# Performance work log

Hardware: AMD Instinct MI355X
Metric: run time of the kernel (lower is better)

The kernel has to match this reference:

```python
import jax, jax.numpy as jnp
import numpy as np

EPS = 1e-8

def _layernorm(x, gamma, beta):
    mu = jnp.mean(x, axis=-1, keepdims=True)
    var = jnp.mean((x - mu) ** 2, axis=-1, keepdims=True)
    return (x - mu) * jax.lax.rsqrt(var + 1e-5) * gamma + beta

def setup_inputs() -> dict:
    key = jax.random.key(0)
    ks = jax.random.split(key, 8)
    B, T, E, H = 64, 512, 512, 2048  # T == E required by original matmul
    s = 1.0 / np.sqrt(E)
    return {
        "x": jax.random.normal(ks[0], (B, T, E), dtype=jnp.float32),
        "gamma1": jnp.ones((E,), jnp.float32),
        "beta1": jnp.zeros((E,), jnp.float32),
        "Wv": jax.random.normal(ks[1], (E, E), jnp.float32) * s,   # surrogate for quantum Vx circuit
        "Ww": jax.random.normal(ks[2], (E, E), jnp.float32) * s,   # surrogate for quantum xWx circuit
        "gamma2": jnp.ones((E,), jnp.float32),
        "beta2": jnp.zeros((E,), jnp.float32),
        "W1": jax.random.normal(ks[3], (E, H), jnp.float32) * s,
        "b1": jnp.zeros((H,), jnp.float32),
        "W2": jax.random.normal(ks[4], (H, E), jnp.float32) * (1.0 / np.sqrt(H)),
        "b2": jnp.zeros((E,), jnp.float32),
    }

def reference(x, gamma1, beta1, Wv, Ww, gamma2, beta2, W1, b1, W2, b2):
    # LN -> quantum-surrogate attention -> residual -> LN -> MLP -> residual
    inp = _layernorm(x, gamma1, beta1)                       # [B,T,E]
    # Quantum Vx surrogate: sampler returns probabilities (non-negative) -> squared projection
    vx = (jnp.einsum('bte,ef->btf', inp, Wv)) ** 2           # [B,T,E], >= 0
    # Quantum xWx surrogate: pairwise bilinear score, squared (probability-like)
    proj = jnp.einsum('bte,ef->btf', inp, Ww)                # [B,T,E]
    xwx = (jnp.einsum('bie,bje->bij', proj, inp)) ** 2       # [B,T,T], >= 0
    vx = jnp.sqrt(vx + EPS)
    xwx = jnp.sqrt(xwx + EPS)
    attn = jax.nn.softmax(xwx, axis=-1)                      # [B,T,T]
    # original: matmul(attn, vx.transpose(1,2)) -> out[b,i,k] = sum_j attn[b,i,j] * vx[b,k,j]
    t = jnp.einsum('bij,bkj->bik', attn, vx)                 # [B,T,T] (T == E)
    x = x + t
    h = _layernorm(x, gamma2, beta2)
    h = jax.nn.gelu(jnp.einsum('bte,eh->bth', h, W1) + b1)
    h = jnp.einsum('bth,he->bte', h, W2) + b2
    return x + h
```

## Files before the change

kernel.cpp:

```cpp
#include <hip/hip_runtime.h>

using f16x8 = __attribute__((ext_vector_type(8))) _Float16;
using f32x4 = __attribute__((ext_vector_type(4))) float;
using u16 = unsigned short;
using u32 = unsigned int;

__device__ __forceinline__ u16 f2h(float f) {
  union { _Float16 h; u16 u; } c;
  c.h = (_Float16)f;
  return c.u;
}
__device__ __forceinline__ uint4 pack8(const u16* h) {
  uint4 r;
  r.x = (u32)h[0] | ((u32)h[1] << 16);
  r.y = (u32)h[2] | ((u32)h[3] << 16);
  r.z = (u32)h[4] | ((u32)h[5] << 16);
  r.w = (u32)h[6] | ((u32)h[7] << 16);
  return r;
}
__device__ __forceinline__ float gelu_fast(float x) {
  float u2 = 1.5957691216057308f * (x + 0.044715f * x * x * x);
  return x / (1.0f + __expf(-u2));
}
__device__ __forceinline__ void gload16(const void* g, void* l) {
  __builtin_amdgcn_global_load_lds(
      (const __attribute__((address_space(1))) void*)g,
      (__attribute__((address_space(3))) void*)l, 16, 0, 0);
}

__global__ __launch_bounds__(256) void transpose_f16_kernel(
    const float* __restrict__ in, u16* __restrict__ out, int R, int C)
{
  __shared__ float t[32][33];
  const int lx = threadIdx.x & 31, ly = threadIdx.x >> 5;
  const int c0 = blockIdx.x << 5, r0 = blockIdx.y << 5;
  for (int i = ly; i < 32; i += 8)
    t[i][lx] = in[(long)(r0 + i) * C + c0 + lx];
  __syncthreads();
  for (int i = ly; i < 32; i += 8)
    out[(long)(c0 + i) * R + r0 + lx] = f2h(t[lx][i]);
}

__global__ __launch_bounds__(256) void ln_f16_kernel(
    const float* __restrict__ x, const float* __restrict__ gamma,
    const float* __restrict__ beta, u16* __restrict__ outH)
{
  const int row  = (blockIdx.x << 2) + (threadIdx.x >> 6);
  const int lane = threadIdx.x & 63;
  const float* xr = x + (long)row * 512 + lane * 8;
  float v[8];
  *(float4*)&v[0] = *(const float4*)xr;
  *(float4*)&v[4] = *(const float4*)(xr + 4);
  float s = 0.f;
#pragma unroll
  for (int j = 0; j < 8; ++j) s += v[j];
#pragma unroll
  for (int o = 32; o; o >>= 1) s += __shfl_xor(s, o);
  const float mu = s * (1.0f / 512.0f);
  float q = 0.f;
#pragma unroll
  for (int j = 0; j < 8; ++j) { float d = v[j] - mu; q += d * d; }
#pragma unroll
  for (int o = 32; o; o >>= 1) q += __shfl_xor(q, o);
  const float rs = rsqrtf(q * (1.0f / 512.0f) + 1e-5f);
  float gv[8], bv[8];
  *(float4*)&gv[0] = *(const float4*)(gamma + lane * 8);
  *(float4*)&gv[4] = *(const float4*)(gamma + lane * 8 + 4);
  *(float4*)&bv[0] = *(const float4*)(beta + lane * 8);
  *(float4*)&bv[4] = *(const float4*)(beta + lane * 8 + 4);
  u16 hs[8];
#pragma unroll
  for (int j = 0; j < 8; ++j)
    hs[j] = f2h((v[j] - mu) * rs * gv[j] + bv[j]);
  *(uint4*)(outH + (long)row * 512 + lane * 8) = pack8(hs);
}

__global__ __launch_bounds__(256) void softmax_kernel(
    const float* __restrict__ scores, u16* __restrict__ attn)
{
  const int row  = (blockIdx.x << 2) + (threadIdx.x >> 6);
  const int lane = threadIdx.x & 63;
  const float* sr = scores + (long)row * 512 + lane * 8;
  float v[8];
  *(float4*)&v[0] = *(const float4*)sr;
  *(float4*)&v[4] = *(const float4*)(sr + 4);
  float m = v[0];
#pragma unroll
  for (int j = 1; j < 8; ++j) m = fmaxf(m, v[j]);
#pragma unroll
  for (int o = 32; o; o >>= 1) m = fmaxf(m, __shfl_xor(m, o));
  float e[8], s = 0.f;
#pragma unroll
  for (int j = 0; j < 8; ++j) { e[j] = __expf(v[j] - m); s += e[j]; }
#pragma unroll
  for (int o = 32; o; o >>= 1) s += __shfl_xor(s, o);
  const float inv = 1.0f / s;
  u16 h[8];
#pragma unroll
  for (int j = 0; j < 8; ++j) h[j] = f2h(e[j] * inv);
  *(uint4*)(attn + (long)row * 512 + lane * 8) = pack8(h);
}

template<int EPI>
__global__ __launch_bounds__(512) void gemm8(
    const char* A0, const char* A1, const char* A2, const char* A3,
    const char* B0, const char* B1, const char* B2, const char* B3,
    int N, int NT, int ldAb, int ldBb,
    long sAb, long sBb, long sC,
    float* __restrict__ outF, u16* __restrict__ outU,
    const float* __restrict__ resid, const float* __restrict__ bias)
{
  __shared__ __align__(16) char lds[131072];
  const int tid = threadIdx.x;
  const int w = tid >> 6, l = tid & 63;
  const int wm = w >> 2, wn = w & 3;

  const int gx = gridDim.x, gy = gridDim.y;
  int flat = ((int)blockIdx.z * gy + (int)blockIdx.y) * gx + (int)blockIdx.x;
  const int total = gx * gy * (int)gridDim.z;
  flat = (flat & 7) * (total >> 3) + (flat >> 3);
  const int bx = flat % gx;
  int rem = flat / gx;
  const int by = rem % gy, bz = rem / gy;

  const long blockM = (long)by * 256;
  const long blockN = (long)bx * 256;
  const long za = (long)bz * sAb;
  const long zb = (long)bz * sBb;
  const char* a0p = A0 + za; const char* a1p = A1 + za;
  const char* a2p = A2 + za; const char* a3p = A3 + za;
  const char* b0p = B0 + zb; const char* b1p = B1 + zb;
  const char* b2p = B2 + zb; const char* b3p = B3 + zb;

  auto partA = [&](int t) { return t < 8 ? a0p : t < 16 ? a1p : t < 24 ? a2p : a3p; };
  auto partB = [&](int t) { return t < 8 ? b0p : t < 16 ? b1p : t < 24 ? b2p : b3p; };

  const long stgSw = ((tid & 7) ^ ((tid >> 3) & 7)) << 4;
  const long raA = (blockM + (tid >> 3)) * (long)ldAb + stgSw;
  const long raB = (blockN + (tid >> 3)) * (long)ldBb + stgSw;
  auto stageA = [&](int t, int h) {
    const char* s = partA(t) + (((long)(t & 7)) << 7) + raA + (long)h * 128 * ldAb;
    char* dptr = lds + ((t & 1) << 15) + (h << 14) + (tid << 4);
    gload16(s, dptr);
    gload16(s + (long)64 * ldAb, dptr + 8192);
  };
  auto stageB = [&](int t, int h) {
    const char* s = partB(t) + (((long)(t & 7)) << 7) + raB + (long)h * 128 * ldBb;
    char* dptr = lds + 65536 + ((t & 1) << 15) + (h << 14) + (tid << 4);
    gload16(s, dptr);
    gload16(s + (long)64 * ldBb, dptr + 8192);
  };

  f32x4 acc[8][4];
#pragma unroll
  for (int i = 0; i < 8; ++i)
#pragma unroll
    for (int j = 0; j < 4; ++j) acc[i][j] = (f32x4){0.f, 0.f, 0.f, 0.f};

  const int lr = l & 15, kg = l >> 4;
  const int xs = kg ^ (l & 7);
  const int po0 = (lr << 7) + (xs << 4);
  const int po1 = (lr << 7) + ((xs ^ 4) << 4);
  const char* aL = lds + (wm << 14);
  const char* bL = lds + 65536 + ((wn >> 1) << 14) + ((wn & 1) << 13);

  f16x8 a[4], bk0[4], bk1[4];
  auto readA = [&](const char* p) {
#pragma unroll
    for (int mf = 0; mf < 4; ++mf) a[mf] = *(const f16x8*)(p + (mf << 11));
  };
  auto readB = [&](f16x8* d, const char* p) {
#pragma unroll
    for (int nf = 0; nf < 4; ++nf) d[nf] = *(const f16x8*)(p + (nf << 11));
  };

#define MFMA16(MH, BK)                                                        \
  do {                                                                        \
    _Pragma("unroll")                                                         \
    for (int mf = 0; mf < 4; ++mf)                                            \
      _Pragma("unroll")                                                       \
      for (int nf = 0; nf < 4; ++nf)                                          \
        acc[MH * 4 + mf][nf] = __builtin_amdgcn_mfma_f32_16x16x32_f16(        \
            BK[nf], a[mf], acc[MH * 4 + mf][nf], 0, 0, 0);                    \
  } while (0)

  stageA(0, 0); stageA(0, 1); stageB(0, 0); stageB(0, 1);
  __syncthreads();

  for (int t = 0; t < NT; ++t) {
    const int d = t & 1;
    const char* aD = aL + (d << 15);
    const char* bD = bL + (d << 15);
    if (t + 1 < NT) {
      stageA(t + 1, 0); stageA(t + 1, 1); stageB(t + 1, 0); stageB(t + 1, 1);
    }
    readA(aD + po0);
    readB(bk0, bD + po0);
    MFMA16(0, bk0);
    readA(aD + po1);
    readB(bk1, bD + po1);
    MFMA16(0, bk1);
    readA(aD + 8192 + po0);
    MFMA16(1, bk0);
    readA(aD + 8192 + po1);
    MFMA16(1, bk1);
    if (t + 1 < NT) __syncthreads();
  }
#undef MFMA16

  const long cb = (long)bz * sC;
  const int m0 = (int)blockM + wm * 128 + lr;
  const int n0 = (int)blockN + wn * 64 + (kg << 2);
#pragma unroll
  for (int mi = 0; mi < 8; ++mi)
#pragma unroll
    for (int ni = 0; ni < 4; ++ni) {
      const int m = m0 + (mi << 4);
      const int n = n0 + (ni << 4);
      const long idx = cb + (long)m * N + n;
      f32x4 v = acc[mi][ni];
      if (EPI == 0) {
        union { u16 h[4]; uint2 u; } p;
#pragma unroll
        for (int r = 0; r < 4; ++r) p.h[r] = f2h(sqrtf(v[r] * v[r] + 1e-8f));
        *(uint2*)(outU + idx) = p.u;
      } else if (EPI == 1) {
        union { u16 h[4]; uint2 u; } p;
#pragma unroll
        for (int r = 0; r < 4; ++r) p.h[r] = f2h(v[r]);
        *(uint2*)(outU + idx) = p.u;
      } else if (EPI == 2) {
        f32x4 o;
#pragma unroll
        for (int r = 0; r < 4; ++r) o[r] = sqrtf(v[r] * v[r] + 1e-8f);
        *(f32x4*)(outF + idx) = o;
      } else if (EPI == 3) {
        f32x4 rd = *(const f32x4*)(resid + idx);
#pragma unroll
        for (int r = 0; r < 4; ++r) rd[r] += v[r];
        *(f32x4*)(outF + idx) = rd;
      } else if (EPI == 4) {
        f32x4 bb = *(const f32x4*)(bias + n);
        union { u16 h[4]; uint2 u; } p;
#pragma unroll
        for (int r = 0; r < 4; ++r) p.h[r] = f2h(gelu_fast(v[r] + bb[r]));
        *(uint2*)(outU + idx) = p.u;
      } else {
        f32x4 rd = *(const f32x4*)(resid + idx);
        f32x4 bb = *(const f32x4*)(bias + n);
#pragma unroll
        for (int r = 0; r < 4; ++r) rd[r] += v[r] + bb[r];
        *(f32x4*)(outF + idx) = rd;
      }
    }
}

extern "C" void kernel_launch(void* const* d_in, const int* in_sizes, int n_in,
                              void* d_out, int out_size, void* d_ws, size_t ws_size,
                              hipStream_t stream)
{
  const float* x   = (const float*)d_in[0];
  const float* g1  = (const float*)d_in[1];
  const float* be1 = (const float*)d_in[2];
  const float* Wv  = (const float*)d_in[3];
  const float* Ww  = (const float*)d_in[4];
  const float* g2  = (const float*)d_in[5];
  const float* be2 = (const float*)d_in[6];
  const float* W1  = (const float*)d_in[7];
  const float* b1  = (const float*)d_in[8];
  const float* W2  = (const float*)d_in[9];
  const float* b2  = (const float*)d_in[10];
  float* out = (float*)d_out;

  char* ws = (char*)d_ws;
  u16* inp    = (u16*)(ws);
  u16* proj   = (u16*)(ws + 33554432);
  float* scores = (float*)(ws + 67108864);
  u16* vx     = (u16*)(ws + 134217728);
  u16* attn   = proj;
  u16* h_in   = inp;
  u16* h_mid  = (u16*)(ws + 33554432);
  char* wb = ws + 167772160;
  u16* WvT = (u16*)(wb);
  u16* WwT = (u16*)(wb + 524288);
  u16* W1T = (u16*)(wb + 1048576);
  u16* W2T = (u16*)(wb + 3145728);

  transpose_f16_kernel<<<dim3(16, 16), 256, 0, stream>>>(Wv, WvT, 512, 512);
  transpose_f16_kernel<<<dim3(16, 16), 256, 0, stream>>>(Ww, WwT, 512, 512);
  transpose_f16_kernel<<<dim3(64, 16), 256, 0, stream>>>(W1, W1T, 512, 2048);
  transpose_f16_kernel<<<dim3(16, 64), 256, 0, stream>>>(W2, W2T, 2048, 512);

  ln_f16_kernel<<<8192, 256, 0, stream>>>(x, g1, be1, inp);

  gemm8<1><<<dim3(2, 128, 1), 512, 0, stream>>>(
      (const char*)inp, (const char*)inp, (const char*)inp, (const char*)inp,
      (const char*)WwT, (const char*)WwT, (const char*)WwT, (const char*)WwT,
      512, 8, 1024, 1024, 0, 0, 0,
      nullptr, proj, nullptr, nullptr);

  gemm8<2><<<dim3(2, 2, 64), 512, 0, stream>>>(
      (const char*)proj, (const char*)proj, (const char*)proj, (const char*)proj,
      (const char*)inp, (const char*)inp, (const char*)inp, (const char*)inp,
      512, 8, 1024, 1024, 524288, 524288, 262144,
      scores, nullptr, nullptr, nullptr);

  softmax_kernel<<<8192, 256, 0, stream>>>(scores, attn);

  gemm8<0><<<dim3(2, 128, 1), 512, 0, stream>>>(
      (const char*)inp, (const char*)inp, (const char*)inp, (const char*)inp,
      (const char*)WvT, (const char*)WvT, (const char*)WvT, (const char*)WvT,
      512, 8, 1024, 1024, 0, 0, 0,
      nullptr, vx, nullptr, nullptr);

  gemm8<3><<<dim3(2, 2, 64), 512, 0, stream>>>(
      (const char*)attn, (const char*)attn, (const char*)attn, (const char*)attn,
      (const char*)vx, (const char*)vx, (const char*)vx, (const char*)vx,
      512, 8, 1024, 1024, 524288, 524288, 262144,
      out, nullptr, x, nullptr);

  ln_f16_kernel<<<8192, 256, 0, stream>>>(out, g2, be2, h_in);

  gemm8<4><<<dim3(8, 128, 1), 512, 0, stream>>>(
      (const char*)h_in, (const char*)h_in, (const char*)h_in, (const char*)h_in,
      (const char*)W1T, (const char*)W1T, (const char*)W1T, (const char*)W1T,
      2048, 8, 1024, 1024, 0, 0, 0,
      nullptr, h_mid, nullptr, b1);

  gemm8<5><<<dim3(2, 128, 1), 512, 0, stream>>>(
      (const char*)h_mid, (const char*)h_mid + 1024, (const char*)h_mid + 2048, (const char*)h_mid + 3072,
      (const char*)W2T, (const char*)W2T + 1024, (const char*)W2T + 2048, (const char*)W2T + 3072,
      512, 32, 4096, 4096, 0, 0, 0,
      out, nullptr, out, b2);
}
```

Measured before the change: 377.3 us.

## Switch GEMM to 32x32x16 MFMA and fuse Ww/Wv projections into one GEMM

Replaces the 16x16x32 MFMA inner loop with 32x32x16 MFMA tiles, which need fewer LDS fragment reads per FLOP. The two separate projection GEMMs (inp·Ww and inp·Wv) become a single N=1024 GEMM over concatenated transposed weights. A new epilogue applies sqrt(x^2+eps) only to the Wv half, and the downstream GEMMs use strided views into the combined buffer. This saves a kernel launch and a second read of inp, but the accumulator and epilogue mapping must exactly match the 32x32 MFMA output layout.

```diff
diff --git a/kernel.cpp b/kernel.cpp
--- a/kernel.cpp
+++ b/kernel.cpp
@@ -1,7 +1,8 @@
 #include <hip/hip_runtime.h>
 
-using f16x8 = __attribute__((ext_vector_type(8))) _Float16;
-using f32x4 = __attribute__((ext_vector_type(4))) float;
+using f16x8  = __attribute__((ext_vector_type(8))) _Float16;
+using f32x4  = __attribute__((ext_vector_type(4))) float;
+using f32x16 = __attribute__((ext_vector_type(16))) float;
 using u16 = unsigned short;
 using u32 = unsigned int;
 
@@ -151,108 +152,99 @@
     gload16(s + (long)64 * ldBb, dptr + 8192);
   };
 
-  f32x4 acc[8][4];
-#pragma unroll
-  for (int i = 0; i < 8; ++i)
-#pragma unroll
-    for (int j = 0; j < 4; ++j) acc[i][j] = (f32x4){0.f, 0.f, 0.f, 0.f};
-
-  const int lr = l & 15, kg = l >> 4;
-  const int xs = kg ^ (l & 7);
-  const int po0 = (lr << 7) + (xs << 4);
-  const int po1 = (lr << 7) + ((xs ^ 4) << 4);
-  const char* aL = lds + (wm << 14);
-  const char* bL = lds + 65536 + ((wn >> 1) << 14) + ((wn & 1) << 13);
-
-  f16x8 a[4], bk0[4], bk1[4];
-  auto readA = [&](const char* p) {
-#pragma unroll
-    for (int mf = 0; mf < 4; ++mf) a[mf] = *(const f16x8*)(p + (mf << 11));
-  };
-  auto readB = [&](f16x8* d, const char* p) {
-#pragma unroll
-    for (int nf = 0; nf < 4; ++nf) d[nf] = *(const f16x8*)(p + (nf << 11));
-  };
-
-#define MFMA16(MH, BK)                                                        \
-  do {                                                                        \
-    _Pragma("unroll")                                                         \
-    for (int mf = 0; mf < 4; ++mf)                                            \
-      _Pragma("unroll")                                                       \
-      for (int nf = 0; nf < 4; ++nf)                                          \
-        acc[MH * 4 + mf][nf] = __builtin_amdgcn_mfma_f32_16x16x32_f16(        \
-            BK[nf], a[mf], acc[MH * 4 + mf][nf], 0, 0, 0);                    \
-  } while (0)
+  f32x16 acc[4][2];
+#pragma unroll
+  for (int i = 0; i < 4; ++i)
+#pragma unroll
+    for (int j = 0; j < 2; ++j)
+#pragma unroll
+      for (int e = 0; e < 16; ++e) acc[i][j][e] = 0.f;
+
+  const int l31 = l & 31, lhi = l >> 5;
+  int sk[4];
+#pragma unroll
+  for (int ks = 0; ks < 4; ++ks)
+    sk[ks] = ((ks * 2 + lhi) ^ (l & 7)) << 4;
+
+  const char* aW = lds + (wm << 14);
+  const char* bW = lds + 65536 + ((wn >> 1) << 14) + ((wn & 1) << 13);
 
   stageA(0, 0); stageA(0, 1); stageB(0, 0); stageB(0, 1);
   __syncthreads();
 
   for (int t = 0; t < NT; ++t) {
     const int d = t & 1;
-    const char* aD = aL + (d << 15);
-    const char* bD = bL + (d << 15);
+    const char* aD = aW + (d << 15);
+    const char* bD = bW + (d << 15);
     if (t + 1 < NT) {
       stageA(t + 1, 0); stageA(t + 1, 1); stageB(t + 1, 0); stageB(t + 1, 1);
     }
-    readA(aD + po0);
-    readB(bk0, bD + po0);
-    MFMA16(0, bk0);
-    readA(aD + po1);
-    readB(bk1, bD + po1);
-    MFMA16(0, bk1);
-    readA(aD + 8192 + po0);
-    MFMA16(1, bk0);
-    readA(aD + 8192 + po1);
-    MFMA16(1, bk1);
+#pragma unroll
+    for (int ks = 0; ks < 4; ++ks) {
+      f16x8 a0 = *(const f16x8*)(aD + ((0 * 32 + l31) << 7) + sk[ks]);
+      f16x8 a1 = *(const f16x8*)(aD + ((1 * 32 + l31) << 7) + sk[ks]);
+      f16x8 a2 = *(const f16x8*)(aD + ((2 * 32 + l31) << 7) + sk[ks]);
+      f16x8 a3 = *(const f16x8*)(aD + ((3 * 32 + l31) << 7) + sk[ks]);
+      f16x8 b0 = *(const f16x8*)(bD + ((0 * 32 + l31) << 7) + sk[ks]);
+      f16x8 b1 = *(const f16x8*)(bD + ((1 * 32 + l31) << 7) + sk[ks]);
+      acc[0][0] = __builtin_amdgcn_mfma_f32_32x32x16_f16(b0, a0, acc[0][0], 0, 0, 0);
+      acc[1][0] = __builtin_amdgcn_mfma_f32_32x32x16_f16(b0, a1, acc[1][0], 0, 0, 0);
+      acc[2][0] = __builtin_amdgcn_mfma_f32_32x32x16_f16(b0, a2, acc[2][0], 0, 0, 0);
+      acc[3][0] = __builtin_amdgcn_mfma_f32_32x32x16_f16(b0, a3, acc[3][0], 0, 0, 0);
+      acc[0][1] = __builtin_amdgcn_mfma_f32_32x32x16_f16(b1, a0, acc[0][1], 0, 0, 0);
+      acc[1][1] = __builtin_amdgcn_mfma_f32_32x32x16_f16(b1, a1, acc[1][1], 0, 0, 0);
+      acc[2][1] = __builtin_amdgcn_mfma_f32_32x32x16_f16(b1, a2, acc[2][1], 0, 0, 0);
+      acc[3][1] = __builtin_amdgcn_mfma_f32_32x32x16_f16(b1, a3, acc[3][1], 0, 0, 0);
+    }
     if (t + 1 < NT) __syncthreads();
   }
-#undef MFMA16
 
   const long cb = (long)bz * sC;
-  const int m0 = (int)blockM + wm * 128 + lr;
-  const int n0 = (int)blockN + wn * 64 + (kg << 2);
-#pragma unroll
-  for (int mi = 0; mi < 8; ++mi)
-#pragma unroll
-    for (int ni = 0; ni < 4; ++ni) {
-      const int m = m0 + (mi << 4);
-      const int n = n0 + (ni << 4);
-      const long idx = cb + (long)m * N + n;
-      f32x4 v = acc[mi][ni];
-      if (EPI == 0) {
-        union { u16 h[4]; uint2 u; } p;
-#pragma unroll
-        for (int r = 0; r < 4; ++r) p.h[r] = f2h(sqrtf(v[r] * v[r] + 1e-8f));
-        *(uint2*)(outU + idx) = p.u;
-      } else if (EPI == 1) {
-        union { u16 h[4]; uint2 u; } p;
-#pragma unroll
-        for (int r = 0; r < 4; ++r) p.h[r] = f2h(v[r]);
-        *(uint2*)(outU + idx) = p.u;
-      } else if (EPI == 2) {
-        f32x4 o;
-#pragma unroll
-        for (int r = 0; r < 4; ++r) o[r] = sqrtf(v[r] * v[r] + 1e-8f);
-        *(f32x4*)(outF + idx) = o;
-      } else if (EPI == 3) {
-        f32x4 rd = *(const f32x4*)(resid + idx);
-#pragma unroll
-        for (int r = 0; r < 4; ++r) rd[r] += v[r];
-        *(f32x4*)(outF + idx) = rd;
-      } else if (EPI == 4) {
-        f32x4 bb = *(const f32x4*)(bias + n);
-        union { u16 h[4]; uint2 u; } p;
-#pragma unroll
-        for (int r = 0; r < 4; ++r) p.h[r] = f2h(gelu_fast(v[r] + bb[r]));
-        *(uint2*)(outU + idx) = p.u;
-      } else {
-        f32x4 rd = *(const f32x4*)(resid + idx);
-        f32x4 bb = *(const f32x4*)(bias + n);
-#pragma unroll
-        for (int r = 0; r < 4; ++r) rd[r] += v[r] + bb[r];
-        *(f32x4*)(outF + idx) = rd;
+  const int m0 = (int)blockM + wm * 128 + l31;
+  const int nb0 = (int)blockN + wn * 64 + (lhi << 2);
+  const bool vabs = (blockN >= 512);
+#pragma unroll
+  for (int mf = 0; mf < 4; ++mf)
+#pragma unroll
+    for (int nf = 0; nf < 2; ++nf)
+#pragma unroll
+      for (int rq = 0; rq < 4; ++rq) {
+        const int m = m0 + mf * 32;
+        const int n = nb0 + nf * 32 + rq * 8;
+        const long idx = cb + (long)m * N + n;
+        f32x4 v;
+#pragma unroll
+        for (int r = 0; r < 4; ++r) v[r] = acc[mf][nf][rq * 4 + r];
+        if (EPI == 2) {
+          f32x4 o;
+#pragma unroll
+          for (int r = 0; r < 4; ++r) o[r] = sqrtf(v[r] * v[r] + 1e-8f);
+          *(f32x4*)(outF + idx) = o;
+        } else if (EPI == 3) {
+          f32x4 rd = *(const f32x4*)(resid + idx);
+#pragma unroll
+          for (int r = 0; r < 4; ++r) rd[r] += v[r];
+          *(f32x4*)(outF + idx) = rd;
+        } else if (EPI == 4) {
+          f32x4 bb = *(const f32x4*)(bias + n);
+          union { u16 h[4]; uint2 u; } p;
+#pragma unroll
+          for (int r = 0; r < 4; ++r) p.h[r] = f2h(gelu_fast(v[r] + bb[r]));
+          *(uint2*)(outU + idx) = p.u;
+        } else if (EPI == 5) {
+          f32x4 rd = *(const f32x4*)(resid + idx);
+          f32x4 bb = *(const f32x4*)(bias + n);
+#pragma unroll
+          for (int r = 0; r < 4; ++r) rd[r] += v[r] + bb[r];
+          *(f32x4*)(outF + idx) = rd;
+        } else {
+          union { u16 h[4]; uint2 u; } p;
+#pragma unroll
+          for (int r = 0; r < 4; ++r)
+            p.h[r] = f2h(vabs ? sqrtf(v[r] * v[r] + 1e-8f) : v[r]);
+          *(uint2*)(outU + idx) = p.u;
+        }
       }
-    }
 }
 
 extern "C" void kernel_launch(void* const* d_in, const int* in_sizes, int n_in,
@@ -274,49 +266,42 @@
 
   char* ws = (char*)d_ws;
   u16* inp    = (u16*)(ws);
-  u16* proj   = (u16*)(ws + 33554432);
-  float* scores = (float*)(ws + 67108864);
-  u16* vx     = (u16*)(ws + 134217728);
-  u16* attn   = proj;
+  u16* pvx    = (u16*)(ws + 33554432);
+  float* scores = (float*)(ws + 100663296);
+  u16* attn   = (u16*)(ws + 167772160);
   u16* h_in   = inp;
   u16* h_mid  = (u16*)(ws + 33554432);
-  char* wb = ws + 167772160;
-  u16* WvT = (u16*)(wb);
-  u16* WwT = (u16*)(wb + 524288);
+  char* wb = ws + 201326592;
+  u16* WwT = (u16*)(wb);
+  u16* WvT = (u16*)(wb + 524288);
   u16* W1T = (u16*)(wb + 1048576);
   u16* W2T = (u16*)(wb + 3145728);
 
+  transpose_f16_kernel<<<dim3(16, 16), 256, 0, stream>>>(Ww, WwT, 512, 512);
   transpose_f16_kernel<<<dim3(16, 16), 256, 0, stream>>>(Wv, WvT, 512, 512);
-  transpose_f16_kernel<<<dim3(16, 16), 256, 0, stream>>>(Ww, WwT, 512, 512);
   transpose_f16_kernel<<<dim3(64, 16), 256, 0, stream>>>(W1, W1T, 512, 2048);
   transpose_f16_kernel<<<dim3(16, 64), 256, 0, stream>>>(W2, W2T, 2048, 512);
 
   ln_f16_kernel<<<8192, 256, 0, stream>>>(x, g1, be1, inp);
 
-  gemm8<1><<<dim3(2, 128, 1), 512, 0, stream>>>(
+  gemm8<6><<<dim3(4, 128, 1), 512, 0, stream>>>(
       (const char*)inp, (const char*)inp, (const char*)inp, (const char*)inp,
       (const char*)WwT, (const char*)WwT, (const char*)WwT, (const char*)WwT,
-      512, 8, 1024, 1024, 0, 0, 0,
-      nullptr, proj, nullptr, nullptr);
+      1024, 8, 1024, 1024, 0, 0, 0,
+      nullptr, pvx, nullptr, nullptr);
 
   gemm8<2><<<dim3(2, 2, 64), 512, 0, stream>>>(
-      (const char*)proj, (const char*)proj, (const char*)proj, (const char*)proj,
+      (const char*)pvx, (const char*)pvx, (const char*)pvx, (const char*)pvx,
       (const char*)inp, (const char*)inp, (const char*)inp, (const char*)inp,
-      512, 8, 1024, 1024, 524288, 524288, 262144,
+      512, 8, 2048, 1024, 1048576, 524288, 262144,
       scores, nullptr, nullptr, nullptr);
 
   softmax_kernel<<<8192, 256, 0, stream>>>(scores, attn);
-
-  gemm8<0><<<dim3(2, 128, 1), 512, 0, stream>>>(
-      (const char*)inp, (const char*)inp, (const char*)inp, (const char*)inp,
-      (const char*)WvT, (const char*)WvT, (const char*)WvT, (const char*)WvT,
-      512, 8, 1024, 1024, 0, 0, 0,
-      nullptr, vx, nullptr, nullptr);
 
   gemm8<3><<<dim3(2, 2, 64), 512, 0, stream>>>(
       (const char*)attn, (const char*)attn, (const char*)attn, (const char*)attn,
-      (const char*)vx, (const char*)vx, (const char*)vx, (const char*)vx,
-      512, 8, 1024, 1024, 524288, 524288, 262144,
+      (const char*)pvx + 1024, (const char*)pvx + 1024, (const char*)pvx + 1024, (const char*)pvx + 1024,
+      512, 8, 1024, 2048, 524288, 1048576, 262144,
       out, nullptr, x, nullptr);
 
   ln_f16_kernel<<<8192, 256, 0, stream>>>(out, g2, be2, h_in);
```

Result: slower. 406.9 us (+7.8%).

## Use 1024-thread GEMM blocks with 16 waves each owning 64x64 tiles

Applied to the files above, without the earlier changes.

The GEMM block grows from 8 to 16 waves while the 256x256 tile stays the same, so each wave now computes a 64x64 sub-tile instead of 128x64. Each thread stages half as many global-to-LDS loads, and per-thread accumulator registers shrink from 32 to 16 fragments. The aim is more latency hiding per CU and lower register pressure. In exchange, A-fragment reuse across the two M halves is lost, and each wave does more LDS reads per MFMA.

```diff
diff --git a/kernel.cpp b/kernel.cpp
--- a/kernel.cpp
+++ b/kernel.cpp
@@ -102,7 +102,7 @@
 }
 
 template<int EPI>
-__global__ __launch_bounds__(512) void gemm8(
+__global__ __launch_bounds__(1024) void gemm8(
     const char* A0, const char* A1, const char* A2, const char* A3,
     const char* B0, const char* B1, const char* B2, const char* B3,
     int N, int NT, int ldAb, int ldBb,
@@ -140,20 +140,16 @@
   const long raB = (blockN + (tid >> 3)) * (long)ldBb + stgSw;
   auto stageA = [&](int t, int h) {
     const char* s = partA(t) + (((long)(t & 7)) << 7) + raA + (long)h * 128 * ldAb;
-    char* dptr = lds + ((t & 1) << 15) + (h << 14) + (tid << 4);
-    gload16(s, dptr);
-    gload16(s + (long)64 * ldAb, dptr + 8192);
+    gload16(s, lds + ((t & 1) << 15) + (h << 14) + (tid << 4));
   };
   auto stageB = [&](int t, int h) {
     const char* s = partB(t) + (((long)(t & 7)) << 7) + raB + (long)h * 128 * ldBb;
-    char* dptr = lds + 65536 + ((t & 1) << 15) + (h << 14) + (tid << 4);
-    gload16(s, dptr);
-    gload16(s + (long)64 * ldBb, dptr + 8192);
+    gload16(s, lds + 65536 + ((t & 1) << 15) + (h << 14) + (tid << 4));
   };
 
-  f32x4 acc[8][4];
-#pragma unroll
-  for (int i = 0; i < 8; ++i)
+  f32x4 acc[4][4];
+#pragma unroll
+  for (int i = 0; i < 4; ++i)
 #pragma unroll
     for (int j = 0; j < 4; ++j) acc[i][j] = (f32x4){0.f, 0.f, 0.f, 0.f};
 
@@ -161,27 +157,27 @@
   const int xs = kg ^ (l & 7);
   const int po0 = (lr << 7) + (xs << 4);
   const int po1 = (lr << 7) + ((xs ^ 4) << 4);
-  const char* aL = lds + (wm << 14);
+  const char* aL = lds + ((wm >> 1) << 14) + ((wm & 1) << 13);
   const char* bL = lds + 65536 + ((wn >> 1) << 14) + ((wn & 1) << 13);
 
-  f16x8 a[4], bk0[4], bk1[4];
+  f16x8 a[4], b[4];
   auto readA = [&](const char* p) {
 #pragma unroll
     for (int mf = 0; mf < 4; ++mf) a[mf] = *(const f16x8*)(p + (mf << 11));
   };
-  auto readB = [&](f16x8* d, const char* p) {
-#pragma unroll
-    for (int nf = 0; nf < 4; ++nf) d[nf] = *(const f16x8*)(p + (nf << 11));
+  auto readB = [&](const char* p) {
+#pragma unroll
+    for (int nf = 0; nf < 4; ++nf) b[nf] = *(const f16x8*)(p + (nf << 11));
   };
 
-#define MFMA16(MH, BK)                                                        \
+#define MFMA16()                                                              \
   do {                                                                        \
     _Pragma("unroll")                                                         \
     for (int mf = 0; mf < 4; ++mf)                                            \
       _Pragma("unroll")                                                       \
       for (int nf = 0; nf < 4; ++nf)                                          \
-        acc[MH * 4 + mf][nf] = __builtin_amdgcn_mfma_f32_16x16x32_f16(        \
-            BK[nf], a[mf], acc[MH * 4 + mf][nf], 0, 0, 0);                    \
+        acc[mf][nf] = __builtin_amdgcn_mfma_f32_16x16x32_f16(                 \
+            b[nf], a[mf], acc[mf][nf], 0, 0, 0);                              \
   } while (0)
 
   stageA(0, 0); stageA(0, 1); stageB(0, 0); stageB(0, 1);
@@ -195,24 +191,20 @@
       stageA(t + 1, 0); stageA(t + 1, 1); stageB(t + 1, 0); stageB(t + 1, 1);
     }
     readA(aD + po0);
-    readB(bk0, bD + po0);
-    MFMA16(0, bk0);
+    readB(bD + po0);
+    MFMA16();
     readA(aD + po1);
-    readB(bk1, bD + po1);
-    MFMA16(0, bk1);
-    readA(aD + 8192 + po0);
-    MFMA16(1, bk0);
-    readA(aD + 8192 + po1);
-    MFMA16(1, bk1);
+    readB(bD + po1);
+    MFMA16();
     if (t + 1 < NT) __syncthreads();
   }
 #undef MFMA16
 
   const long cb = (long)bz * sC;
-  const int m0 = (int)blockM + wm * 128 + lr;
+  const int m0 = (int)blockM + wm * 64 + lr;
   const int n0 = (int)blockN + wn * 64 + (kg << 2);
 #pragma unroll
-  for (int mi = 0; mi < 8; ++mi)
+  for (int mi = 0; mi < 4; ++mi)
 #pragma unroll
     for (int ni = 0; ni < 4; ++ni) {
       const int m = m0 + (mi << 4);
@@ -293,13 +285,13 @@
 
   ln_f16_kernel<<<8192, 256, 0, stream>>>(x, g1, be1, inp);
 
-  gemm8<1><<<dim3(2, 128, 1), 512, 0, stream>>>(
+  gemm8<1><<<dim3(2, 128, 1), 1024, 0, stream>>>(
       (const char*)inp, (const char*)inp, (const char*)inp, (const char*)inp,
       (const char*)WwT, (const char*)WwT, (const char*)WwT, (const char*)WwT,
       512, 8, 1024, 1024, 0, 0, 0,
       nullptr, proj, nullptr, nullptr);
 
-  gemm8<2><<<dim3(2, 2, 64), 512, 0, stream>>>(
+  gemm8<2><<<dim3(2, 2, 64), 1024, 0, stream>>>(
       (const char*)proj, (const char*)proj, (const char*)proj, (const char*)proj,
       (const char*)inp, (const char*)inp, (const char*)inp, (const char*)inp,
       512, 8, 1024, 1024, 524288, 524288, 262144,
@@ -307,13 +299,13 @@
 
   softmax_kernel<<<8192, 256, 0, stream>>>(scores, attn);
 
-  gemm8<0><<<dim3(2, 128, 1), 512, 0, stream>>>(
+  gemm8<0><<<dim3(2, 128, 1), 1024, 0, stream>>>(
       (const char*)inp, (const char*)inp, (const char*)inp, (const char*)inp,
       (const char*)WvT, (const char*)WvT, (const char*)WvT, (const char*)WvT,
       512, 8, 1024, 1024, 0, 0, 0,
       nullptr, vx, nullptr, nullptr);
 
-  gemm8<3><<<dim3(2, 2, 64), 512, 0, stream>>>(
+  gemm8<3><<<dim3(2, 2, 64), 1024, 0, stream>>>(
       (const char*)attn, (const char*)attn, (const char*)attn, (const char*)attn,
       (const char*)vx, (const char*)vx, (const char*)vx, (const char*)vx,
       512, 8, 1024, 1024, 524288, 524288, 262144,
@@ -321,13 +313,13 @@
 
   ln_f16_kernel<<<8192, 256, 0, stream>>>(out, g2, be2, h_in);
 
-  gemm8<4><<<dim3(8, 128, 1), 512, 0, stream>>>(
+  gemm8<4><<<dim3(8, 128, 1), 1024, 0, stream>>>(
       (const char*)h_in, (const char*)h_in, (const char*)h_in, (const char*)h_in,
       (const char*)W1T, (const char*)W1T, (const char*)W1T, (const char*)W1T,
       2048, 8, 1024, 1024, 0, 0, 0,
       nullptr, h_mid, nullptr, b1);
 
-  gemm8<5><<<dim3(2, 128, 1), 512, 0, stream>>>(
+  gemm8<5><<<dim3(2, 128, 1), 1024, 0, stream>>>(
       (const char*)h_mid, (const char*)h_mid + 1024, (const char*)h_mid + 2048, (const char*)h_mid + 3072,
       (const char*)W2T, (const char*)W2T + 1024, (const char*)W2T + 2048, (const char*)W2T + 3072,
       512, 32, 4096, 4096, 0, 0, 0,
```

After: 368.8 us. 1.02x faster.
